# Kernel optimization log

Hardware: AMD Instinct MI355X
Metric: run time of the kernel (lower is better)

## Reference

```python
import jax, jax.numpy as jnp
import numpy as np

EPS = 1e-8
M_MARGIN = 0.5  # circle-loss margin m


def _l2norm(x):
    # torch.cosine_similarity clamps the norm product at eps; clamping each norm is equivalent in effect for randn data
    return x / jnp.maximum(jnp.linalg.norm(x, axis=-1, keepdims=True), EPS)


def setup_inputs() -> dict:
    key = jax.random.key(0)
    k1, k2, k3, k4 = jax.random.split(key, 4)
    N, D = 8192, 1024
    return {
        "text_embeddings": jax.random.normal(k1, (N, D), dtype=jnp.float32),
        "text_pos_embeddings": jax.random.normal(k2, (N, D), dtype=jnp.float32),
        "text_neg_embeddings": jax.random.normal(k3, (N, D), dtype=jnp.float32),
        "text_neg_index": jax.random.randint(k4, (N,), 0, N, dtype=jnp.int64 if jax.config.jax_enable_x64 else jnp.int32),
    }


def reference(text_embeddings, text_pos_embeddings, text_neg_embeddings, text_neg_index):
    # use_all_pair=False, mixcse=-1 branch of RetriContrastLoss.forward
    q = _l2norm(text_embeddings)        # [N, D]
    p = _l2norm(text_pos_embeddings)    # [N, D]
    n = _l2norm(text_neg_embeddings)    # [M, D]

    # normalize-then-GEMM == cosine_similarity(unsqueeze(1), unsqueeze(0))
    sim_neg = jnp.einsum("nd,md->nm", q, n)       # [N, M] query-vs-neg cosines
    sim_pos = jnp.sum(q * p, axis=-1)             # [N]    query-vs-pos diagonal cosines
    # NOTE: temperature is never applied in this branch (faithful to source)

    m = M_MARGIN
    # negatives: an = clamp_min(detach(s) + (1+m), 0); s' = an * (s - delta_n), delta_n = -(1-m)
    an = jnp.maximum(jax.lax.stop_gradient(sim_neg) + (1.0 + m), 0.0)
    s_neg = an * (sim_neg + (1.0 - m))
    # positives: ap = clamp_min(-detach(s) + (1+m), 0); s' = -ap * (s - delta_p), delta_p = 1-m
    ap = jnp.maximum(-jax.lax.stop_gradient(sim_pos) + (1.0 + m), 0.0)
    s_pos = -ap * (sim_pos - (1.0 - m))

    # source flattens via boolean mask then logsumexp over dim=0 -> global logsumexp
    lse_neg = jax.scipy.special.logsumexp(s_neg.reshape(-1))
    lse_pos = jax.scipy.special.logsumexp(s_pos)
    return jax.nn.softplus(lse_neg + lse_pos)
```

## Files before the change

kernel.cpp:

```cpp
#include <hip/hip_runtime.h>
#include <hip/hip_bf16.h>
#include <hip/hip_fp8.h>

#define D_K 1024
#define TILE 128
#define ROWB 512
#define KB_ITER 128

typedef int intx8 __attribute__((ext_vector_type(8)));
typedef float floatx4 __attribute__((ext_vector_type(4)));

__device__ __forceinline__ unsigned int f2fp4(float v) {
    const float a = fabsf(v);
    unsigned int c = (unsigned int)(a >= 0.25f) + (a >= 0.75f) + (a >= 1.25f)
                   + (a >= 1.75f) + (a >= 2.5f) + (a >= 3.5f) + (a >= 5.0f);
    return c | (v < 0.0f ? 8u : 0u);
}

__device__ __forceinline__ void gl_lds16(const void* g, void* l) {
    __builtin_amdgcn_global_load_lds(
        (const __attribute__((address_space(1))) unsigned int*)g,
        (__attribute__((address_space(3))) unsigned int*)l,
        16, 0, 0);
}

__device__ __forceinline__ intx8 ld_frag4(const unsigned char* rowbase, int c, int e) {
    const int4 d = *(const int4*)(rowbase + ((c ^ e) * 16));
    intx8 v;
    v[0] = d.x; v[1] = d.y; v[2] = d.z; v[3] = d.w;
    v[4] = 0; v[5] = 0; v[6] = 0; v[7] = 0;
    return v;
}

__global__ __launch_bounds__(256)
void prep_kernel(const float* __restrict__ q, const float* __restrict__ p,
                 const float* __restrict__ ng,
                 unsigned short* __restrict__ qn, unsigned short* __restrict__ nn,
                 float* __restrict__ posp) {
    const int wid = threadIdx.x >> 6, lane = threadIdx.x & 63;
    const int row = blockIdx.x * 4 + wid;
    const size_t base = (size_t)row * D_K;
    const float4* q4 = (const float4*)(q + base);
    const float4* p4 = (const float4*)(p + base);
    const float4* n4 = (const float4*)(ng + base);

    float4 qa[4], na[4];
    float qq = 0.f, pp = 0.f, qp = 0.f, nn2 = 0.f;
#pragma unroll
    for (int j = 0; j < 4; j++) {
        qa[j] = q4[j * 64 + lane];
        float4 pa = p4[j * 64 + lane];
        na[j] = n4[j * 64 + lane];
        qq += qa[j].x*qa[j].x + qa[j].y*qa[j].y + qa[j].z*qa[j].z + qa[j].w*qa[j].w;
        pp += pa.x*pa.x + pa.y*pa.y + pa.z*pa.z + pa.w*pa.w;
        qp += qa[j].x*pa.x + qa[j].y*pa.y + qa[j].z*pa.z + qa[j].w*pa.w;
        nn2 += na[j].x*na[j].x + na[j].y*na[j].y + na[j].z*na[j].z + na[j].w*na[j].w;
    }
#pragma unroll
    for (int off = 1; off < 64; off <<= 1) {
        qq += __shfl_xor(qq, off);
        pp += __shfl_xor(pp, off);
        qp += __shfl_xor(qp, off);
        nn2 += __shfl_xor(nn2, off);
    }
    const float rq = 32.0f / fmaxf(sqrtf(qq), 1e-8f);
    const float rn = 32.0f / fmaxf(sqrtf(nn2), 1e-8f);

    unsigned short* qr = qn + (size_t)row * 256;
    unsigned short* nr = nn + (size_t)row * 256;
#pragma unroll
    for (int j = 0; j < 4; j++) {
        unsigned int w = f2fp4(qa[j].x * rq) | (f2fp4(qa[j].y * rq) << 4)
                       | (f2fp4(qa[j].z * rq) << 8) | (f2fp4(qa[j].w * rq) << 12);
        qr[j * 64 + lane] = (unsigned short)w;
        w = f2fp4(na[j].x * rn) | (f2fp4(na[j].y * rn) << 4)
          | (f2fp4(na[j].z * rn) << 8) | (f2fp4(na[j].w * rn) << 12);
        nr[j * 64 + lane] = (unsigned short)w;
    }

    if (lane == 0) {
        const float rp = 1.0f / fmaxf(sqrtf(pp), 1e-8f);
        const float sim = qp * (rq / 32.0f) * rp;
        const float ap = fmaxf(1.5f - sim, 0.0f);
        const float sp = -ap * (sim - 0.5f);
        posp[row] = __expf(sp - 4.0f);
    }
}

__global__ __launch_bounds__(256, 2)
void gemm_lse_fp4(const unsigned char* __restrict__ A,
                  const unsigned char* __restrict__ B,
                  float* __restrict__ negp) {
    __shared__ unsigned char As[TILE * KB_ITER];
    __shared__ unsigned char Bs[TILE * KB_ITER];

    const int tid = threadIdx.x;
    const int wid = tid >> 6;
    const int lane = tid & 63;
    const int tile_m = blockIdx.y * TILE;
    const int tile_n = blockIdx.x * TILE;

    const int wave_m = (wid & 1) * 64;
    const int wave_n = (wid >> 1) * 64;
    const int quad = lane >> 4;
    const int r = lane & 15;
    const int e = r & 7;

    floatx4 acc[4][4] = {};

    int lds_off[4];
    size_t src_off[4];
#pragma unroll
    for (int s = 0; s < 4; s++) {
        const int cc = s * 256 + tid;
        const int row = cc >> 3, slot = cc & 7;
        lds_off[s] = cc * 16;
        src_off[s] = (size_t)row * ROWB + (size_t)((slot ^ (row & 7)) * 16);
    }
    const unsigned char* Ab = A + (size_t)tile_m * ROWB;
    const unsigned char* Bb = B + (size_t)tile_n * ROWB;

    for (int k0b = 0; k0b < ROWB; k0b += KB_ITER) {
#pragma unroll
        for (int s = 0; s < 4; s++) {
            gl_lds16(Ab + src_off[s] + k0b, &As[lds_off[s]]);
            gl_lds16(Bb + src_off[s] + k0b, &Bs[lds_off[s]]);
        }
        __syncthreads();

#pragma unroll
        for (int t = 0; t < 2; t++) {
            intx8 a[4], b[4];
#pragma unroll
            for (int i = 0; i < 4; i++)
                a[i] = ld_frag4(&As[(wave_m + i * 16 + r) * KB_ITER], t * 4 + quad, e);
#pragma unroll
            for (int j = 0; j < 4; j++)
                b[j] = ld_frag4(&Bs[(wave_n + j * 16 + r) * KB_ITER], t * 4 + quad, e);

#pragma unroll
            for (int i = 0; i < 4; i++)
#pragma unroll
                for (int j = 0; j < 4; j++)
                    acc[i][j] = __builtin_amdgcn_mfma_scale_f32_16x16x128_f8f6f4(
                        a[i], b[j], acc[i][j],
                        4, 4,
                        0, 0x7A7A7A7A,
                        0, 0x7A7A7A7A);
        }

        __syncthreads();
    }

    float lsum = 0.0f;
#pragma unroll
    for (int i = 0; i < 4; i++)
#pragma unroll
        for (int j = 0; j < 4; j++)
#pragma unroll
            for (int el = 0; el < 4; el++) {
                const float s = acc[i][j][el];
                const float an = fmaxf(s + 1.5f, 0.0f);
                const float sn = an * (s + 0.5f);
                lsum += __expf(sn - 4.0f);
            }
    for (int off = 32; off > 0; off >>= 1) lsum += __shfl_down(lsum, off);
    __shared__ float red[4];
    if (lane == 0) red[wid] = lsum;
    __syncthreads();
    if (tid == 0)
        negp[blockIdx.y * gridDim.x + blockIdx.x] = red[0] + red[1] + red[2] + red[3];
}

__global__ __launch_bounds__(1024)
void finalize_kernel(const float* __restrict__ negp, int n_neg,
                     const float* __restrict__ posp, int n_pos,
                     float* __restrict__ out) {
    double sn = 0.0, sp = 0.0;
    for (int i = threadIdx.x; i < n_neg; i += 1024) sn += (double)negp[i];
    for (int i = threadIdx.x; i < n_pos; i += 1024) sp += (double)posp[i];
    for (int off = 32; off > 0; off >>= 1) {
        sn += __shfl_down(sn, off);
        sp += __shfl_down(sp, off);
    }
    __shared__ double rn[16], rp[16];
    const int wid = threadIdx.x >> 6, lane = threadIdx.x & 63;
    if (lane == 0) { rn[wid] = sn; rp[wid] = sp; }
    __syncthreads();
    if (threadIdx.x == 0) {
        double NS = 0.0, PS = 0.0;
#pragma unroll
        for (int w = 0; w < 16; w++) { NS += rn[w]; PS += rp[w]; }
        const double x = (4.0 + log(NS)) + (4.0 + log(PS));
        const double spl = (x > 30.0) ? x : log1p(exp(x));
        out[0] = (float)spl;
    }
}

extern "C" void kernel_launch(void* const* d_in, const int* in_sizes, int n_in,
                              void* d_out, int out_size, void* d_ws, size_t ws_size,
                              hipStream_t stream) {
    const float* q = (const float*)d_in[0];
    const float* p = (const float*)d_in[1];
    const float* ng = (const float*)d_in[2];

    const int N = in_sizes[3];
    const int D = in_sizes[0] / N;
    const int M = in_sizes[2] / D;

    char* ws = (char*)d_ws;
    unsigned short* qn = (unsigned short*)ws;
    unsigned short* nn = (unsigned short*)(ws + (size_t)N * ROWB);
    float* negp = (float*)(ws + (size_t)(N + M) * ROWB);
    const int n_neg = (M / TILE) * (N / TILE);
    float* posp = negp + n_neg;

    prep_kernel<<<N / 4, 256, 0, stream>>>(q, p, ng, qn, nn, posp);
    gemm_lse_fp4<<<dim3(M / TILE, N / TILE), 256, 0, stream>>>(
        (const unsigned char*)qn, (const unsigned char*)nn, negp);
    finalize_kernel<<<1, 1024, 0, stream>>>(negp, n_neg, posp, N, (float*)d_out);
}
```

Baseline: 163.2 us.

## Load FP4 GEMM fragments directly from global memory, dropping LDS staging

```diff
diff --git a/kernel.cpp b/kernel.cpp
--- a/kernel.cpp
+++ b/kernel.cpp
@@ -5,7 +5,6 @@
 #define D_K 1024
 #define TILE 128
 #define ROWB 512
-#define KB_ITER 128
 
 typedef int intx8 __attribute__((ext_vector_type(8)));
 typedef float floatx4 __attribute__((ext_vector_type(4)));
@@ -17,15 +16,8 @@
     return c | (v < 0.0f ? 8u : 0u);
 }
 
-__device__ __forceinline__ void gl_lds16(const void* g, void* l) {
-    __builtin_amdgcn_global_load_lds(
-        (const __attribute__((address_space(1))) unsigned int*)g,
-        (__attribute__((address_space(3))) unsigned int*)l,
-        16, 0, 0);
-}
-
-__device__ __forceinline__ intx8 ld_frag4(const unsigned char* rowbase, int c, int e) {
-    const int4 d = *(const int4*)(rowbase + ((c ^ e) * 16));
+__device__ __forceinline__ intx8 ld_g16(const unsigned char* p) {
+    const int4 d = *(const int4*)p;
     intx8 v;
     v[0] = d.x; v[1] = d.y; v[2] = d.z; v[3] = d.w;
     v[4] = 0; v[5] = 0; v[6] = 0; v[7] = 0;
@@ -91,9 +83,6 @@
 void gemm_lse_fp4(const unsigned char* __restrict__ A,
                   const unsigned char* __restrict__ B,
                   float* __restrict__ negp) {
-    __shared__ unsigned char As[TILE * KB_ITER];
-    __shared__ unsigned char Bs[TILE * KB_ITER];
-
     const int tid = threadIdx.x;
     const int wid = tid >> 6;
     const int lane = tid & 63;
@@ -104,52 +93,34 @@
     const int wave_n = (wid >> 1) * 64;
     const int quad = lane >> 4;
     const int r = lane & 15;
-    const int e = r & 7;
 
     floatx4 acc[4][4] = {};
 
-    int lds_off[4];
-    size_t src_off[4];
+    const unsigned char* pa[4];
+    const unsigned char* pb[4];
 #pragma unroll
-    for (int s = 0; s < 4; s++) {
-        const int cc = s * 256 + tid;
-        const int row = cc >> 3, slot = cc & 7;
-        lds_off[s] = cc * 16;
-        src_off[s] = (size_t)row * ROWB + (size_t)((slot ^ (row & 7)) * 16);
+    for (int i = 0; i < 4; i++) {
+        pa[i] = A + (size_t)(tile_m + wave_m + i * 16 + r) * ROWB + quad * 16;
+        pb[i] = B + (size_t)(tile_n + wave_n + i * 16 + r) * ROWB + quad * 16;
     }
-    const unsigned char* Ab = A + (size_t)tile_m * ROWB;
-    const unsigned char* Bb = B + (size_t)tile_n * ROWB;
-
-    for (int k0b = 0; k0b < ROWB; k0b += KB_ITER) {
-#pragma unroll
-        for (int s = 0; s < 4; s++) {
-            gl_lds16(Ab + src_off[s] + k0b, &As[lds_off[s]]);
-            gl_lds16(Bb + src_off[s] + k0b, &Bs[lds_off[s]]);
-        }
-        __syncthreads();
 
 #pragma unroll
-        for (int t = 0; t < 2; t++) {
-            intx8 a[4], b[4];
+    for (int kk = 0; kk < 8; kk++) {
+        intx8 a[4], b[4];
 #pragma unroll
-            for (int i = 0; i < 4; i++)
-                a[i] = ld_frag4(&As[(wave_m + i * 16 + r) * KB_ITER], t * 4 + quad, e);
+        for (int i = 0; i < 4; i++) a[i] = ld_g16(pa[i] + kk * 64);
+#pragma unroll
+        for (int j = 0; j < 4; j++) b[j] = ld_g16(pb[j] + kk * 64);
+
+#pragma unroll
+        for (int i = 0; i < 4; i++)
 #pragma unroll
             for (int j = 0; j < 4; j++)
-                b[j] = ld_frag4(&Bs[(wave_n + j * 16 + r) * KB_ITER], t * 4 + quad, e);
-
-#pragma unroll
-            for (int i = 0; i < 4; i++)
-#pragma unroll
-                for (int j = 0; j < 4; j++)
-                    acc[i][j] = __builtin_amdgcn_mfma_scale_f32_16x16x128_f8f6f4(
-                        a[i], b[j], acc[i][j],
-                        4, 4,
-                        0, 0x7A7A7A7A,
-                        0, 0x7A7A7A7A);
-        }
-
-        __syncthreads();
+                acc[i][j] = __builtin_amdgcn_mfma_scale_f32_16x16x128_f8f6f4(
+                    a[i], b[j], acc[i][j],
+                    4, 4,
+                    0, 0x7A7A7A7A,
+                    0, 0x7A7A7A7A);
     }
 
     float lsum = 0.0f;
```

Measured after the change: 241.4 us. 47.9% more time.
